# Optimization experiments

Measured on AMD Instinct MI355X. Metric: run time of the kernel, lower is better.

Reference implementation:

```python
import jax, jax.numpy as jnp
import numpy as np

NUM_HEADS = 6
DIM = 384            # internal attention dim (MultiHeadAttention default)
IN_DIM = 768
HIDDEN = 3072        # int(in_dim * mlp_ratio)
EPS = 1e-5


def _ln(x, w, b):
    m = x.mean(-1, keepdims=True)
    v = ((x - m) ** 2).mean(-1, keepdims=True)
    return (x - m) / jnp.sqrt(v + EPS) * w + b


def _mha(q_in, c_in, Wq, Wkv, Wp, bp):
    # q_in: [b, n, IN_DIM], c_in: [b, m, IN_DIM]
    b, n, _ = q_in.shape
    m = c_in.shape[1]
    h, d = NUM_HEADS, DIM // NUM_HEADS
    scale = d ** -0.5
    q = (q_in @ Wq).reshape(b, n, h, d)
    kv = (c_in @ Wkv).reshape(b, m, 2, h, d)
    k, v = kv[:, :, 0], kv[:, :, 1]
    attn = jax.nn.softmax(jnp.einsum('bnhd,bmhd->bhnm', q, k) * scale, axis=-1)
    out = jnp.einsum('bhnm,bmhd->bnhd', attn, v).reshape(b, n, DIM)
    return out @ Wp + bp


def _mlp(x, W1, b1, W2, b2):
    return jax.nn.gelu(x @ W1 + b1, approximate=False) @ W2 + b2


def setup_inputs() -> dict:
    key = jax.random.key(0)
    ks = jax.random.split(key, 16)
    s = 0.02
    inp = {
        'query': jax.random.normal(ks[0], (8, 1024, IN_DIM), jnp.float32),
        'context': jax.random.normal(ks[1], (8, 2048, IN_DIM), jnp.float32),
        'ln_w': jnp.ones((IN_DIM,), jnp.float32),
        'ln_b': jnp.zeros((IN_DIM,), jnp.float32),
        'a1_wq': jax.random.normal(ks[2], (IN_DIM, DIM), jnp.float32) * s,
        'a1_wkv': jax.random.normal(ks[3], (IN_DIM, 2 * DIM), jnp.float32) * s,
        'a1_wp': jax.random.normal(ks[4], (DIM, IN_DIM), jnp.float32) * s,
        'a1_bp': jnp.zeros((IN_DIM,), jnp.float32),
        'm1_w1': jax.random.normal(ks[5], (IN_DIM, HIDDEN), jnp.float32) * s,
        'm1_b1': jnp.zeros((HIDDEN,), jnp.float32),
        'm1_w2': jax.random.normal(ks[6], (HIDDEN, IN_DIM), jnp.float32) * s,
        'm1_b2': jnp.zeros((IN_DIM,), jnp.float32),
        'a2_wq': jax.random.normal(ks[7], (IN_DIM, DIM), jnp.float32) * s,
        'a2_wkv': jax.random.normal(ks[8], (IN_DIM, 2 * DIM), jnp.float32) * s,
        'a2_wp': jax.random.normal(ks[9], (DIM, IN_DIM), jnp.float32) * s,
        'a2_bp': jnp.zeros((IN_DIM,), jnp.float32),
        'm2_w1': jax.random.normal(ks[10], (IN_DIM, HIDDEN), jnp.float32) * s,
        'm2_b1': jnp.zeros((HIDDEN,), jnp.float32),
        'm2_w2': jax.random.normal(ks[11], (HIDDEN, IN_DIM), jnp.float32) * s,
        'm2_b2': jnp.zeros((IN_DIM,), jnp.float32),
    }
    return inp


def reference(query, context, ln_w, ln_b,
              a1_wq, a1_wkv, a1_wp, a1_bp,
              m1_w1, m1_b1, m1_w2, m1_b2,
              a2_wq, a2_wkv, a2_wp, a2_bp,
              m2_w1, m2_b1, m2_w2, m2_b2):
    q = _ln(query, ln_w, ln_b)                                   # [b, nq, in_dim]
    c = _mha(q, _ln(context, ln_w, ln_b), a1_wq, a1_wkv, a1_wp, a1_bp)  # [b, nq, in_dim]
    c = c + _mlp(_ln(c, ln_w, ln_b), m1_w1, m1_b1, m1_w2, m1_b2)
    c = c + _mha(q, _ln(c, ln_w, ln_b), a2_wq, a2_wkv, a2_wp, a2_bp)
    c = c + _mlp(_ln(c, ln_w, ln_b), m2_w1, m2_b1, m2_w2, m2_b2)
    return (c, q)
```

## Files before the change

kernel.cpp:

```cpp
#include <hip/hip_runtime.h>
#include <hip/hip_bf16.h>
#include <math.h>

typedef unsigned short u16;
typedef __bf16 bf16x8 __attribute__((ext_vector_type(8)));
typedef short s16x4 __attribute__((ext_vector_type(4)));
typedef float f32x4 __attribute__((ext_vector_type(4)));

#define B_   8
#define NQ   1024
#define NC   2048
#define IND  768
#define DIM  384
#define NH   6
#define HD   64
#define HID  3072

__device__ __forceinline__ u16 f2b(float f){
  unsigned int x = __float_as_uint(f);
  return (u16)((x + 0x7fffu + ((x >> 16) & 1u)) >> 16);
}

__device__ __forceinline__ void gl_lds16(const u16* g, u16* l){
  __builtin_amdgcn_global_load_lds(
    (const __attribute__((address_space(1))) unsigned int*)g,
    (__attribute__((address_space(3))) unsigned int*)l, 16, 0, 0);
}

__global__ void wtrans_kernel(const float* __restrict__ W, u16* __restrict__ Wt,
                              int K, int N){
  __shared__ float tile[32][33];
  int n0 = blockIdx.x * 32, k0 = blockIdx.y * 32;
  int tx = threadIdx.x, ty = threadIdx.y;
  #pragma unroll
  for(int i=0;i<4;i++) tile[ty*4+i][tx] = W[(size_t)(k0+ty*4+i)*N + n0 + tx];
  __syncthreads();
  #pragma unroll
  for(int i=0;i<4;i++) Wt[(size_t)(n0+ty*4+i)*K + k0 + tx] = f2b(tile[tx][ty*4+i]);
}

__global__ void vtrans_kernel(const u16* __restrict__ KV, u16* __restrict__ Vt, int M){
  __shared__ u16 t[64][72];
  int bh = blockIdx.y; int b = bh / NH, h = bh % NH;
  int m0 = blockIdx.x * 64;
  int tx = threadIdx.x & 63, ty = threadIdx.x >> 6;
  #pragma unroll
  for(int i=0;i<16;i++){
    int mm = ty*16+i;
    t[mm][tx] = KV[(size_t)(b*M + m0 + mm)*(2*DIM) + DIM + h*HD + tx];
  }
  __syncthreads();
  #pragma unroll
  for(int i=0;i<16;i++){
    int dd = ty*16+i;
    Vt[(size_t)(bh*HD + dd)*M + m0 + tx] = t[tx][dd];
  }
}

template<bool ALSO_F32>
__global__ void ln_kernel(const float* __restrict__ x, const float* __restrict__ w,
                          const float* __restrict__ bia, u16* __restrict__ yb,
                          float* __restrict__ yf){
  int row = blockIdx.x;
  const float* xr = x + (size_t)row * IND;
  int t = threadIdx.x;
  float v[3];
  v[0] = xr[t]; v[1] = xr[t+256]; v[2] = xr[t+512];
  float s  = v[0]+v[1]+v[2];
  float sq = v[0]*v[0]+v[1]*v[1]+v[2]*v[2];
  #pragma unroll
  for(int o=1;o<64;o<<=1){ s += __shfl_xor(s, o, 64); sq += __shfl_xor(sq, o, 64); }
  __shared__ float ss[4], ssq[4];
  int wid = t >> 6;
  if((t&63)==0){ ss[wid]=s; ssq[wid]=sq; }
  __syncthreads();
  s  = ss[0]+ss[1]+ss[2]+ss[3];
  sq = ssq[0]+ssq[1]+ssq[2]+ssq[3];
  float mean = s * (1.0f/IND);
  float var  = sq * (1.0f/IND) - mean*mean;
  float rs   = rsqrtf(var + 1e-5f);
  #pragma unroll
  for(int i=0;i<3;i++){
    int idx = t + i*256;
    float y = (v[i]-mean)*rs*w[idx] + bia[idx];
    yb[(size_t)row*IND + idx] = f2b(y);
    if(ALSO_F32) yf[(size_t)row*IND + idx] = y;
  }
}

template<int OUTM, bool BIAS, bool GELU_>
__global__ __launch_bounds__(256) void gemm_bt(const u16* __restrict__ A,
    const u16* __restrict__ Wt, const float* __restrict__ bias,
    void* __restrict__ C, int K, int N){
  __shared__ __align__(16) u16 As[128][32];
  __shared__ __align__(16) u16 Bs[128][32];
  int rowblk = blockIdx.x * 128, colblk = blockIdx.y * 128;
  int tid = threadIdx.x;
  int lane = tid & 63, wv = tid >> 6;
  int wm = (wv >> 1) * 64, wn = (wv & 1) * 64;
  int l16 = lane & 15, quad = lane >> 4;
  f32x4 acc[4][4] = {};
  int sr = lane >> 2, sc = (lane & 3) * 8;
  const u16* Ap = A  + (size_t)(rowblk + wv*16 + sr) * K + sc;
  const u16* Bp = Wt + (size_t)(colblk + wv*16 + sr) * K + sc;
  u16* lA0 = &As[wv*16][0];      u16* lA1 = &As[64 + wv*16][0];
  u16* lB0 = &Bs[wv*16][0];      u16* lB1 = &Bs[64 + wv*16][0];
  for(int kt = 0; kt < K; kt += 32){
    gl_lds16(Ap + kt,                 lA0);
    gl_lds16(Ap + (size_t)64*K + kt,  lA1);
    gl_lds16(Bp + kt,                 lB0);
    gl_lds16(Bp + (size_t)64*K + kt,  lB1);
    __syncthreads();
    bf16x8 af[4], bfr[4];
    #pragma unroll
    for(int i=0;i<4;i++) af[i]  = *(const bf16x8*)&As[wm + i*16 + l16][quad*8];
    #pragma unroll
    for(int j=0;j<4;j++) bfr[j] = *(const bf16x8*)&Bs[wn + j*16 + l16][quad*8];
    #pragma unroll
    for(int i=0;i<4;i++)
      #pragma unroll
      for(int j=0;j<4;j++)
        acc[i][j] = __builtin_amdgcn_mfma_f32_16x16x32_bf16(af[i], bfr[j], acc[i][j], 0, 0, 0);
    __syncthreads();
  }
  #pragma unroll
  for(int i=0;i<4;i++){
    #pragma unroll
    for(int j=0;j<4;j++){
      int grow = rowblk + wm + i*16 + quad*4;
      int gcol = colblk + wn + j*16 + l16;
      float bv = BIAS ? bias[gcol] : 0.0f;
      #pragma unroll
      for(int rg=0; rg<4; rg++){
        float vval = acc[i][j][rg] + bv;
        if(GELU_) vval = 0.5f * vval * (1.0f + erff(vval * 0.70710678118f));
        size_t idx = (size_t)(grow + rg) * N + gcol;
        if(OUTM == 0)      ((u16*)C)[idx]   = f2b(vval);
        else if(OUTM == 1) ((float*)C)[idx] = vval;
        else               ((float*)C)[idx] += vval;
      }
    }
  }
}

__global__ __launch_bounds__(256) void attn_kernel(const u16* __restrict__ Q,
    const u16* __restrict__ KV, const u16* __restrict__ Vtg,
    u16* __restrict__ AO, int M){
  __shared__ __align__(16) u16 Ks[128][68];
  __shared__ __align__(16) u16 Vs[64][132];
  int tid = threadIdx.x, lane = tid & 63, wv = tid >> 6;
  int qt = blockIdx.x & (NQ/64 - 1);
  int bh = blockIdx.x >> 4;
  int h = bh % NH, b = bh / NH;
  int l16 = lane & 15, quad = lane >> 4;
  const float sc2 = 0.18033688011f;

  s16x4 qf[4];
  const u16* qp = Q + (size_t)(b*NQ + qt*64 + wv*16 + l16) * DIM + h*HD + quad*4;
  #pragma unroll
  for(int s=0;s<4;s++) qf[s] = *(const s16x4*)(qp + s*16);

  f32x4 o[4] = {};
  float lacc = 0.f;

  for(int cb = 0; cb < M; cb += 128){
    __syncthreads();
    #pragma unroll
    for(int it=0; it<4; it++){
      int idx = tid + it*256;
      int row = idx >> 3, c8 = (idx & 7) * 8;
      *(int4*)&Ks[row][c8] =
        *(const int4*)(KV + (size_t)(b*M + cb + row)*(2*DIM) + h*HD + c8);
    }
    #pragma unroll
    for(int it=0; it<4; it++){
      int idx = tid + it*256;
      int dd = idx >> 4, c8 = (idx & 15) * 8;
      *(int4*)&Vs[dd][c8] =
        *(const int4*)(Vtg + (size_t)(bh*HD + dd)*M + cb + c8);
    }
    __syncthreads();

    s16x4 pp[8];
    #pragma unroll
    for(int cc=0; cc<8; cc++){
      f32x4 z = {};
      #pragma unroll
      for(int s=0;s<4;s++){
        s16x4 kf = *(const s16x4*)&Ks[cc*16 + l16][quad*4 + s*16];
        z = __builtin_amdgcn_mfma_f32_16x16x16bf16_1k(kf, qf[s], z, 0,0,0);
      }
      f32x4 p;
      #pragma unroll
      for(int j=0;j<4;j++) p[j] = exp2f(z[j]*sc2);
      lacc += (p[0]+p[1]) + (p[2]+p[3]);
      s16x4 pb;
      #pragma unroll
      for(int j=0;j<4;j++) pb[j] = (short)f2b(p[j]);
      pp[cc] = pb;
    }
    #pragma unroll
    for(int dn=0;dn<4;dn++){
      #pragma unroll
      for(int t=0;t<8;t++){
        s16x4 vf = *(const s16x4*)&Vs[dn*16 + l16][quad*4 + t*16];
        o[dn] = __builtin_amdgcn_mfma_f32_16x16x16bf16_1k(vf, pp[t], o[dn], 0,0,0);
      }
    }
  }

  lacc += __shfl_xor(lacc, 16, 64);
  lacc += __shfl_xor(lacc, 32, 64);
  float rl = 1.0f / lacc;

  u16* aop = AO + (size_t)(b*NQ + qt*64 + wv*16 + l16) * DIM + h*HD + quad*4;
  #pragma unroll
  for(int dn=0;dn<4;dn++){
    s16x4 ob;
    #pragma unroll
    for(int r=0;r<4;r++) ob[r] = (short)f2b(o[dn][r] * rl);
    *(s16x4*)(aop + dn*16) = ob;
  }
}

extern "C" void kernel_launch(void* const* d_in, const int* in_sizes, int n_in,
                              void* d_out, int out_size, void* d_ws, size_t ws_size,
                              hipStream_t stream){
  const float* query   = (const float*)d_in[0];
  const float* context = (const float*)d_in[1];
  const float* ln_w  = (const float*)d_in[2];
  const float* ln_b  = (const float*)d_in[3];
  const float* a1_wq = (const float*)d_in[4];
  const float* a1_wkv= (const float*)d_in[5];
  const float* a1_wp = (const float*)d_in[6];
  const float* a1_bp = (const float*)d_in[7];
  const float* m1_w1 = (const float*)d_in[8];
  const float* m1_b1 = (const float*)d_in[9];
  const float* m1_w2 = (const float*)d_in[10];
  const float* m1_b2 = (const float*)d_in[11];
  const float* a2_wq = (const float*)d_in[12];
  const float* a2_wkv= (const float*)d_in[13];
  const float* a2_wp = (const float*)d_in[14];
  const float* a2_bp = (const float*)d_in[15];
  const float* m2_w1 = (const float*)d_in[16];
  const float* m2_b1 = (const float*)d_in[17];
  const float* m2_w2 = (const float*)d_in[18];
  const float* m2_b2 = (const float*)d_in[19];
  (void)in_sizes; (void)n_in; (void)out_size; (void)ws_size;

  float* c_out = (float*)d_out;
  float* q_out = c_out + (size_t)B_*NQ*IND;

  char* base = (char*)d_ws;
  size_t off = 0;
  auto alloc = [&](size_t elems)->u16*{
    u16* p = (u16*)(base + off);
    off += ((elems*2) + 255) & ~(size_t)255;
    return p;
  };
  u16* wq1t  = alloc((size_t)DIM*IND);
  u16* wkv1t = alloc((size_t)2*DIM*IND);
  u16* wp1t  = alloc((size_t)IND*DIM);
  u16* w11t  = alloc((size_t)HID*IND);
  u16* w21t  = alloc((size_t)IND*HID);
  u16* wq2t  = alloc((size_t)DIM*IND);
  u16* wkv2t = alloc((size_t)2*DIM*IND);
  u16* wp2t  = alloc((size_t)IND*DIM);
  u16* w12t  = alloc((size_t)HID*IND);
  u16* w22t  = alloc((size_t)IND*HID);
  u16* qn_b  = alloc((size_t)B_*NQ*IND);
  u16* cn_b  = alloc((size_t)B_*NC*IND);
  u16* Tb    = alloc((size_t)B_*NQ*IND);
  u16* Qb    = alloc((size_t)B_*NQ*DIM);
  u16* KVb   = alloc((size_t)B_*NC*2*DIM);
  u16* AOb   = alloc((size_t)B_*NQ*DIM);
  u16* Hb    = alloc((size_t)B_*NQ*HID);
  u16* Vtb   = Hb;

  dim3 tb(32,8);
  wtrans_kernel<<<dim3(DIM/32,   IND/32), tb, 0, stream>>>(a1_wq,  wq1t,  IND, DIM);
  wtrans_kernel<<<dim3(2*DIM/32, IND/32), tb, 0, stream>>>(a1_wkv, wkv1t, IND, 2*DIM);
  wtrans_kernel<<<dim3(IND/32,   DIM/32), tb, 0, stream>>>(a1_wp,  wp1t,  DIM, IND);
  wtrans_kernel<<<dim3(HID/32,   IND/32), tb, 0, stream>>>(m1_w1,  w11t,  IND, HID);
  wtrans_kernel<<<dim3(IND/32,   HID/32), tb, 0, stream>>>(m1_w2,  w21t,  HID, IND);
  wtrans_kernel<<<dim3(DIM/32,   IND/32), tb, 0, stream>>>(a2_wq,  wq2t,  IND, DIM);
  wtrans_kernel<<<dim3(2*DIM/32, IND/32), tb, 0, stream>>>(a2_wkv, wkv2t, IND, 2*DIM);
  wtrans_kernel<<<dim3(IND/32,   DIM/32), tb, 0, stream>>>(a2_wp,  wp2t,  DIM, IND);
  wtrans_kernel<<<dim3(HID/32,   IND/32), tb, 0, stream>>>(m2_w1,  w12t,  IND, HID);
  wtrans_kernel<<<dim3(IND/32,   HID/32), tb, 0, stream>>>(m2_w2,  w22t,  HID, IND);

  ln_kernel<true ><<<B_*NQ, 256, 0, stream>>>(query,   ln_w, ln_b, qn_b, q_out);
  ln_kernel<false><<<B_*NC, 256, 0, stream>>>(context, ln_w, ln_b, cn_b, nullptr);

  gemm_bt<0,false,false><<<dim3(B_*NQ/128, DIM/128),   256, 0, stream>>>(qn_b, wq1t,  nullptr, Qb,  IND, DIM);
  gemm_bt<0,false,false><<<dim3(B_*NC/128, 2*DIM/128), 256, 0, stream>>>(cn_b, wkv1t, nullptr, KVb, IND, 2*DIM);
  vtrans_kernel<<<dim3(NC/64, B_*NH), 256, 0, stream>>>(KVb, Vtb, NC);
  attn_kernel<<<B_*NH*(NQ/64), 256, 0, stream>>>(Qb, KVb, Vtb, AOb, NC);
  gemm_bt<1,true,false><<<dim3(B_*NQ/128, IND/128), 256, 0, stream>>>(AOb, wp1t, a1_bp, c_out, DIM, IND);
  ln_kernel<false><<<B_*NQ, 256, 0, stream>>>(c_out, ln_w, ln_b, Tb, nullptr);
  gemm_bt<0,true,true ><<<dim3(B_*NQ/128, HID/128), 256, 0, stream>>>(Tb, w11t, m1_b1, Hb, IND, HID);
  gemm_bt<2,true,false><<<dim3(B_*NQ/128, IND/128), 256, 0, stream>>>(Hb, w21t, m1_b2, c_out, HID, IND);
  ln_kernel<false><<<B_*NQ, 256, 0, stream>>>(c_out, ln_w, ln_b, Tb, nullptr);
  gemm_bt<0,false,false><<<dim3(B_*NQ/128, DIM/128),   256, 0, stream>>>(qn_b, wq2t,  nullptr, Qb,  IND, DIM);
  gemm_bt<0,false,false><<<dim3(B_*NQ/128, 2*DIM/128), 256, 0, stream>>>(Tb,   wkv2t, nullptr, KVb, IND, 2*DIM);
  vtrans_kernel<<<dim3(NQ/64, B_*NH), 256, 0, stream>>>(KVb, Vtb, NQ);
  attn_kernel<<<B_*NH*(NQ/64), 256, 0, stream>>>(Qb, KVb, Vtb, AOb, NQ);
  gemm_bt<2,true,false><<<dim3(B_*NQ/128, IND/128), 256, 0, stream>>>(AOb, wp2t, a2_bp, c_out, DIM, IND);
  ln_kernel<false><<<B_*NQ, 256, 0, stream>>>(c_out, ln_w, ln_b, Tb, nullptr);
  gemm_bt<0,true,true ><<<dim3(B_*NQ/128, HID/128), 256, 0, stream>>>(Tb, w12t, m2_b1, Hb, IND, HID);
  gemm_bt<2,true,false><<<dim3(B_*NQ/128, IND/128), 256, 0, stream>>>(Hb, w22t, m2_b2, c_out, HID, IND);
}
```

Measured before the change: 854.5 us.

## Split-K the narrow-output GEMMs with atomic accumulation into the residual

Adds a K-split mode to the GEMM that uses the z grid dimension, so each block handles one slice of K and atomically adds its partial result into the fp32 output. Only the split-0 block adds the bias. The attention-projection GEMMs (split 2) and MLP down-projection GEMMs (split 4) switch to this mode, and the first projection now zeroes its output with a memset beforehand. This targets the low block count of the 768-wide-output GEMMs (64x6 blocks) and the long serial K loop of the K=3072 GEMMs. The cost is atomic traffic on the output, an extra memset, and a float summation order that is no longer deterministic.

```diff
diff --git a/kernel.cpp b/kernel.cpp
--- a/kernel.cpp
+++ b/kernel.cpp
@@ -91,25 +91,26 @@
 template<int OUTM, bool BIAS, bool GELU_>
 __global__ __launch_bounds__(256) void gemm_bt(const u16* __restrict__ A,
     const u16* __restrict__ Wt, const float* __restrict__ bias,
-    void* __restrict__ C, int K, int N){
+    void* __restrict__ C, int Kstr, int Kc, int N){
   __shared__ __align__(16) u16 As[128][32];
   __shared__ __align__(16) u16 Bs[128][32];
   int rowblk = blockIdx.x * 128, colblk = blockIdx.y * 128;
+  int kbase = blockIdx.z * Kc;
   int tid = threadIdx.x;
   int lane = tid & 63, wv = tid >> 6;
   int wm = (wv >> 1) * 64, wn = (wv & 1) * 64;
   int l16 = lane & 15, quad = lane >> 4;
   f32x4 acc[4][4] = {};
   int sr = lane >> 2, sc = (lane & 3) * 8;
-  const u16* Ap = A  + (size_t)(rowblk + wv*16 + sr) * K + sc;
-  const u16* Bp = Wt + (size_t)(colblk + wv*16 + sr) * K + sc;
+  const u16* Ap = A  + (size_t)(rowblk + wv*16 + sr) * Kstr + kbase + sc;
+  const u16* Bp = Wt + (size_t)(colblk + wv*16 + sr) * Kstr + kbase + sc;
   u16* lA0 = &As[wv*16][0];      u16* lA1 = &As[64 + wv*16][0];
   u16* lB0 = &Bs[wv*16][0];      u16* lB1 = &Bs[64 + wv*16][0];
-  for(int kt = 0; kt < K; kt += 32){
-    gl_lds16(Ap + kt,                 lA0);
-    gl_lds16(Ap + (size_t)64*K + kt,  lA1);
-    gl_lds16(Bp + kt,                 lB0);
-    gl_lds16(Bp + (size_t)64*K + kt,  lB1);
+  for(int kt = 0; kt < Kc; kt += 32){
+    gl_lds16(Ap + kt,                    lA0);
+    gl_lds16(Ap + (size_t)64*Kstr + kt,  lA1);
+    gl_lds16(Bp + kt,                    lB0);
+    gl_lds16(Bp + (size_t)64*Kstr + kt,  lB1);
     __syncthreads();
     bf16x8 af[4], bfr[4];
     #pragma unroll
@@ -123,13 +124,14 @@
         acc[i][j] = __builtin_amdgcn_mfma_f32_16x16x32_bf16(af[i], bfr[j], acc[i][j], 0, 0, 0);
     __syncthreads();
   }
+  bool addb = BIAS && (OUTM != 3 || blockIdx.z == 0);
   #pragma unroll
   for(int i=0;i<4;i++){
     #pragma unroll
     for(int j=0;j<4;j++){
       int grow = rowblk + wm + i*16 + quad*4;
       int gcol = colblk + wn + j*16 + l16;
-      float bv = BIAS ? bias[gcol] : 0.0f;
+      float bv = addb ? bias[gcol] : 0.0f;
       #pragma unroll
       for(int rg=0; rg<4; rg++){
         float vval = acc[i][j][rg] + bv;
@@ -137,7 +139,8 @@
         size_t idx = (size_t)(grow + rg) * N + gcol;
         if(OUTM == 0)      ((u16*)C)[idx]   = f2b(vval);
         else if(OUTM == 1) ((float*)C)[idx] = vval;
-        else               ((float*)C)[idx] += vval;
+        else if(OUTM == 2) ((float*)C)[idx] += vval;
+        else               atomicAdd(&((float*)C)[idx], vval);
       }
     }
   }
@@ -292,21 +295,22 @@
   ln_kernel<true ><<<B_*NQ, 256, 0, stream>>>(query,   ln_w, ln_b, qn_b, q_out);
   ln_kernel<false><<<B_*NC, 256, 0, stream>>>(context, ln_w, ln_b, cn_b, nullptr);
 
-  gemm_bt<0,false,false><<<dim3(B_*NQ/128, DIM/128),   256, 0, stream>>>(qn_b, wq1t,  nullptr, Qb,  IND, DIM);
-  gemm_bt<0,false,false><<<dim3(B_*NC/128, 2*DIM/128), 256, 0, stream>>>(cn_b, wkv1t, nullptr, KVb, IND, 2*DIM);
+  gemm_bt<0,false,false><<<dim3(B_*NQ/128, DIM/128),   256, 0, stream>>>(qn_b, wq1t,  nullptr, Qb,  IND, IND, DIM);
+  gemm_bt<0,false,false><<<dim3(B_*NC/128, 2*DIM/128), 256, 0, stream>>>(cn_b, wkv1t, nullptr, KVb, IND, IND, 2*DIM);
   vtrans_kernel<<<dim3(NC/64, B_*NH), 256, 0, stream>>>(KVb, Vtb, NC);
   attn_kernel<<<B_*NH*(NQ/64), 256, 0, stream>>>(Qb, KVb, Vtb, AOb, NC);
-  gemm_bt<1,true,false><<<dim3(B_*NQ/128, IND/128), 256, 0, stream>>>(AOb, wp1t, a1_bp, c_out, DIM, IND);
+  hipMemsetAsync(c_out, 0, (size_t)B_*NQ*IND*sizeof(float), stream);
+  gemm_bt<3,true,false><<<dim3(B_*NQ/128, IND/128, 2), 256, 0, stream>>>(AOb, wp1t, a1_bp, c_out, DIM, DIM/2, IND);
   ln_kernel<false><<<B_*NQ, 256, 0, stream>>>(c_out, ln_w, ln_b, Tb, nullptr);
-  gemm_bt<0,true,true ><<<dim3(B_*NQ/128, HID/128), 256, 0, stream>>>(Tb, w11t, m1_b1, Hb, IND, HID);
-  gemm_bt<2,true,false><<<dim3(B_*NQ/128, IND/128), 256, 0, stream>>>(Hb, w21t, m1_b2, c_out, HID, IND);
+  gemm_bt<0,true,true ><<<dim3(B_*NQ/128, HID/128), 256, 0, stream>>>(Tb, w11t, m1_b1, Hb, IND, IND, HID);
+  gemm_bt<3,true,false><<<dim3(B_*NQ/128, IND/128, 4), 256, 0, stream>>>(Hb, w21t, m1_b2, c_out, HID, HID/4, IND);
   ln_kernel<false><<<B_*NQ, 256, 0, stream>>>(c_out, ln_w, ln_b, Tb, nullptr);
-  gemm_bt<0,false,false><<<dim3(B_*NQ/128, DIM/128),   256, 0, stream>>>(qn_b, wq2t,  nullptr, Qb,  IND, DIM);
-  gemm_bt<0,false,false><<<dim3(B_*NQ/128, 2*DIM/128), 256, 0, stream>>>(Tb,   wkv2t, nullptr, KVb, IND, 2*DIM);
+  gemm_bt<0,false,false><<<dim3(B_*NQ/128, DIM/128),   256, 0, stream>>>(qn_b, wq2t,  nullptr, Qb,  IND, IND, DIM);
+  gemm_bt<0,false,false><<<dim3(B_*NQ/128, 2*DIM/128), 256, 0, stream>>>(Tb,   wkv2t, nullptr, KVb, IND, IND, 2*DIM);
   vtrans_kernel<<<dim3(NQ/64, B_*NH), 256, 0, stream>>>(KVb, Vtb, NQ);
   attn_kernel<<<B_*NH*(NQ/64), 256, 0, stream>>>(Qb, KVb, Vtb, AOb, NQ);
-  gemm_bt<2,true,false><<<dim3(B_*NQ/128, IND/128), 256, 0, stream>>>(AOb, wp2t, a2_bp, c_out, DIM, IND);
+  gemm_bt<3,true,false><<<dim3(B_*NQ/128, IND/128, 2), 256, 0, stream>>>(AOb, wp2t, a2_bp, c_out, DIM, DIM/2, IND);
   ln_kernel<false><<<B_*NQ, 256, 0, stream>>>(c_out, ln_w, ln_b, Tb, nullptr);
-  gemm_bt<0,true,true ><<<dim3(B_*NQ/128, HID/128), 256, 0, stream>>>(Tb, w12t, m2_b1, Hb, IND, HID);
-  gemm_bt<2,true,false><<<dim3(B_*NQ/128, IND/128), 256, 0, stream>>>(Hb, w22t, m2_b2, c_out, HID, IND);
-}
+  gemm_bt<0,true,true ><<<dim3(B_*NQ/128, HID/128), 256, 0, stream>>>(Tb, w12t, m2_b1, Hb, IND, IND, HID);
+  gemm_bt<3,true,false><<<dim3(B_*NQ/128, IND/128, 4), 256, 0, stream>>>(Hb, w22t, m2_b2, c_out, HID, HID/4, IND);
+}
```

Result: slower. 946.9 us (+10.8%).

## Add narrow GEMM N-tile option, XOR-swizzle LDS, and reorder attention block mapping

Applied to the files above, without the earlier changes.

The GEMM is templated on its N tile width. The small-N projections (Q, output, MLP down, second KV) now use 64-wide tiles to launch more blocks and fill the GPU better. LDS loads and fragment reads use an XOR swizzle on the 8-element column group to reduce bank conflicts. The attention grid index now puts batch-head in the fast dimension, changing block scheduling order and locality. Narrower tiles lower per-block arithmetic intensity and increase redundant A-tile loads.

```diff
diff --git a/kernel.cpp b/kernel.cpp
--- a/kernel.cpp
+++ b/kernel.cpp
@@ -88,45 +88,50 @@
   }
 }
 
-template<int OUTM, bool BIAS, bool GELU_>
+template<int TN, int OUTM, bool BIAS, bool GELU_>
 __global__ __launch_bounds__(256) void gemm_bt(const u16* __restrict__ A,
     const u16* __restrict__ Wt, const float* __restrict__ bias,
     void* __restrict__ C, int K, int N){
+  constexpr int JT = TN / 32;
   __shared__ __align__(16) u16 As[128][32];
-  __shared__ __align__(16) u16 Bs[128][32];
-  int rowblk = blockIdx.x * 128, colblk = blockIdx.y * 128;
+  __shared__ __align__(16) u16 Bs[TN][32];
+  int rowblk = blockIdx.x * 128, colblk = blockIdx.y * TN;
   int tid = threadIdx.x;
   int lane = tid & 63, wv = tid >> 6;
-  int wm = (wv >> 1) * 64, wn = (wv & 1) * 64;
+  int wm = (wv >> 1) * 64, wn = (wv & 1) * (16*JT);
   int l16 = lane & 15, quad = lane >> 4;
-  f32x4 acc[4][4] = {};
-  int sr = lane >> 2, sc = (lane & 3) * 8;
+  f32x4 acc[4][JT] = {};
+  int sr = lane >> 2;
+  int sc = (((lane & 3) ^ ((lane >> 3) & 3)) * 8);
+  int rc = ((quad ^ ((l16 >> 1) & 3)) * 8);
   const u16* Ap = A  + (size_t)(rowblk + wv*16 + sr) * K + sc;
   const u16* Bp = Wt + (size_t)(colblk + wv*16 + sr) * K + sc;
   u16* lA0 = &As[wv*16][0];      u16* lA1 = &As[64 + wv*16][0];
-  u16* lB0 = &Bs[wv*16][0];      u16* lB1 = &Bs[64 + wv*16][0];
+  u16* lB0 = &Bs[wv*16][0];
   for(int kt = 0; kt < K; kt += 32){
     gl_lds16(Ap + kt,                 lA0);
     gl_lds16(Ap + (size_t)64*K + kt,  lA1);
     gl_lds16(Bp + kt,                 lB0);
-    gl_lds16(Bp + (size_t)64*K + kt,  lB1);
+    if(TN == 128){
+      gl_lds16(Bp + (size_t)64*K + kt, &Bs[0][0] + (64 + wv*16)*32);
+    }
     __syncthreads();
-    bf16x8 af[4], bfr[4];
-    #pragma unroll
-    for(int i=0;i<4;i++) af[i]  = *(const bf16x8*)&As[wm + i*16 + l16][quad*8];
-    #pragma unroll
-    for(int j=0;j<4;j++) bfr[j] = *(const bf16x8*)&Bs[wn + j*16 + l16][quad*8];
+    bf16x8 af[4], bfr[JT];
+    #pragma unroll
+    for(int i=0;i<4;i++)  af[i]  = *(const bf16x8*)&As[wm + i*16 + l16][rc];
+    #pragma unroll
+    for(int j=0;j<JT;j++) bfr[j] = *(const bf16x8*)&Bs[wn + j*16 + l16][rc];
     #pragma unroll
     for(int i=0;i<4;i++)
       #pragma unroll
-      for(int j=0;j<4;j++)
+      for(int j=0;j<JT;j++)
         acc[i][j] = __builtin_amdgcn_mfma_f32_16x16x32_bf16(af[i], bfr[j], acc[i][j], 0, 0, 0);
     __syncthreads();
   }
   #pragma unroll
   for(int i=0;i<4;i++){
     #pragma unroll
-    for(int j=0;j<4;j++){
+    for(int j=0;j<JT;j++){
       int grow = rowblk + wm + i*16 + quad*4;
       int gcol = colblk + wn + j*16 + l16;
       float bv = BIAS ? bias[gcol] : 0.0f;
@@ -149,8 +154,8 @@
   __shared__ __align__(16) u16 Ks[128][68];
   __shared__ __align__(16) u16 Vs[64][132];
   int tid = threadIdx.x, lane = tid & 63, wv = tid >> 6;
-  int qt = blockIdx.x & (NQ/64 - 1);
-  int bh = blockIdx.x >> 4;
+  int bh = blockIdx.x % (B_*NH);
+  int qt = blockIdx.x / (B_*NH);
   int h = bh % NH, b = bh / NH;
   int l16 = lane & 15, quad = lane >> 4;
   const float sc2 = 0.18033688011f;
@@ -292,21 +297,21 @@
   ln_kernel<true ><<<B_*NQ, 256, 0, stream>>>(query,   ln_w, ln_b, qn_b, q_out);
   ln_kernel<false><<<B_*NC, 256, 0, stream>>>(context, ln_w, ln_b, cn_b, nullptr);
 
-  gemm_bt<0,false,false><<<dim3(B_*NQ/128, DIM/128),   256, 0, stream>>>(qn_b, wq1t,  nullptr, Qb,  IND, DIM);
-  gemm_bt<0,false,false><<<dim3(B_*NC/128, 2*DIM/128), 256, 0, stream>>>(cn_b, wkv1t, nullptr, KVb, IND, 2*DIM);
+  gemm_bt<64,0,false,false><<<dim3(B_*NQ/128, DIM/64),  256, 0, stream>>>(qn_b, wq1t,  nullptr, Qb,  IND, DIM);
+  gemm_bt<128,0,false,false><<<dim3(B_*NC/128, 2*DIM/128), 256, 0, stream>>>(cn_b, wkv1t, nullptr, KVb, IND, 2*DIM);
   vtrans_kernel<<<dim3(NC/64, B_*NH), 256, 0, stream>>>(KVb, Vtb, NC);
   attn_kernel<<<B_*NH*(NQ/64), 256, 0, stream>>>(Qb, KVb, Vtb, AOb, NC);
-  gemm_bt<1,true,false><<<dim3(B_*NQ/128, IND/128), 256, 0, stream>>>(AOb, wp1t, a1_bp, c_out, DIM, IND);
+  gemm_bt<64,1,true,false><<<dim3(B_*NQ/128, IND/64), 256, 0, stream>>>(AOb, wp1t, a1_bp, c_out, DIM, IND);
   ln_kernel<false><<<B_*NQ, 256, 0, stream>>>(c_out, ln_w, ln_b, Tb, nullptr);
-  gemm_bt<0,true,true ><<<dim3(B_*NQ/128, HID/128), 256, 0, stream>>>(Tb, w11t, m1_b1, Hb, IND, HID);
-  gemm_bt<2,true,false><<<dim3(B_*NQ/128, IND/128), 256, 0, stream>>>(Hb, w21t, m1_b2, c_out, HID, IND);
+  gemm_bt<128,0,true,true ><<<dim3(B_*NQ/128, HID/128), 256, 0, stream>>>(Tb, w11t, m1_b1, Hb, IND, HID);
+  gemm_bt<64,2,true,false><<<dim3(B_*NQ/128, IND/64), 256, 0, stream>>>(Hb, w21t, m1_b2, c_out, HID, IND);
   ln_kernel<false><<<B_*NQ, 256, 0, stream>>>(c_out, ln_w, ln_b, Tb, nullptr);
-  gemm_bt<0,false,false><<<dim3(B_*NQ/128, DIM/128),   256, 0, stream>>>(qn_b, wq2t,  nullptr, Qb,  IND, DIM);
-  gemm_bt<0,false,false><<<dim3(B_*NQ/128, 2*DIM/128), 256, 0, stream>>>(Tb,   wkv2t, nullptr, KVb, IND, 2*DIM);
+  gemm_bt<64,0,false,false><<<dim3(B_*NQ/128, DIM/64),  256, 0, stream>>>(qn_b, wq2t,  nullptr, Qb,  IND, DIM);
+  gemm_bt<64,0,false,false><<<dim3(B_*NQ/128, 2*DIM/64), 256, 0, stream>>>(Tb,   wkv2t, nullptr, KVb, IND, 2*DIM);
   vtrans_kernel<<<dim3(NQ/64, B_*NH), 256, 0, stream>>>(KVb, Vtb, NQ);
   attn_kernel<<<B_*NH*(NQ/64), 256, 0, stream>>>(Qb, KVb, Vtb, AOb, NQ);
-  gemm_bt<2,true,false><<<dim3(B_*NQ/128, IND/128), 256, 0, stream>>>(AOb, wp2t, a2_bp, c_out, DIM, IND);
+  gemm_bt<64,2,true,false><<<dim3(B_*NQ/128, IND/64), 256, 0, stream>>>(AOb, wp2t, a2_bp, c_out, DIM, IND);
   ln_kernel<false><<<B_*NQ, 256, 0, stream>>>(c_out, ln_w, ln_b, Tb, nullptr);
-  gemm_bt<0,true,true ><<<dim3(B_*NQ/128, HID/128), 256, 0, stream>>>(Tb, w12t, m2_b1, Hb, IND, HID);
-  gemm_bt<2,true,false><<<dim3(B_*NQ/128, IND/128), 256, 0, stream>>>(Hb, w22t, m2_b2, c_out, HID, IND);
-}
+  gemm_bt<128,0,true,true ><<<dim3(B_*NQ/128, HID/128), 256, 0, stream>>>(Tb, w12t, m2_b1, Hb, IND, HID);
+  gemm_bt<64,2,true,false><<<dim3(B_*NQ/128, IND/64), 256, 0, stream>>>(Hb, w22t, m2_b2, c_out, HID, IND);
+}
```

Result: faster. 767.1 us (-10.2%).
